# Kernel tuning notes

Hardware: AMD Instinct MI355X
Metric: run time of the kernel (lower is better)

The kernel has to match this reference:

```python
import jax, jax.numpy as jnp
import numpy as np

N = 50000   # nodes
E = 400000  # edges
H = 128     # num_hidden


def _glorot(key, shape):
    fan_in, fan_out = shape
    lim = float(np.sqrt(6.0 / (fan_in + fan_out)))
    return jax.random.uniform(key, shape, jnp.float32, -lim, lim)


def setup_inputs() -> dict:
    key = jax.random.key(0)
    ks = jax.random.split(key, 16)
    x = jax.random.normal(ks[0], (N, H), jnp.float32)
    pos = jax.random.normal(ks[1], (N, 3), jnp.float32)
    pe = jax.random.normal(ks[2], (N, H), jnp.float32)
    send = jax.random.randint(ks[3], (E,), 0, N)
    # avoid self-loops so dist > 0 (torch.norm grad at 0 is NaN; same hazard in jax)
    off = jax.random.randint(ks[4], (E,), 1, N)
    rec = (send + off) % N
    edge_index = jnp.stack([send, rec]).astype(jnp.int64)
    # message_mlp: Linear(4H+1, H) -> SiLU -> Linear(H, H) -> SiLU
    W1 = _glorot(ks[5], (4 * H + 1, H)); b1 = jnp.zeros((H,), jnp.float32)
    W2 = _glorot(ks[6], (H, H));          b2 = jnp.zeros((H,), jnp.float32)
    # message_mlp_pos: Linear(2H+1, H) -> Tanh -> Linear(H, H) -> Tanh
    Wp1 = _glorot(ks[7], (2 * H + 1, H)); bp1 = jnp.zeros((H,), jnp.float32)
    Wp2 = _glorot(ks[8], (H, H));          bp2 = jnp.zeros((H,), jnp.float32)
    return {"x": x, "pos": pos, "pe": pe, "edge_index": edge_index,
            "W1": W1, "b1": b1, "W2": W2, "b2": b2,
            "Wp1": Wp1, "bp1": bp1, "Wp2": Wp2, "bp2": bp2}


def reference(x, pos, pe, edge_index, W1, b1, W2, b2, Wp1, bp1, Wp2, bp2):
    send, rec = edge_index[0], edge_index[1]
    # gather node + pe features along edges
    dist = jnp.linalg.norm(pos[send] - pos[rec], axis=1, keepdims=True)  # [E,1]
    state = jnp.concatenate([x[send], pe[send], x[rec], pe[rec], dist], axis=1)  # [E,4H+1]
    state_pe = jnp.concatenate([pe[send], pe[rec], dist], axis=1)                 # [E,2H+1]
    # edge MLPs
    msg = jax.nn.silu(jax.nn.silu(state @ W1 + b1) @ W2 + b2)      # [E,H]
    msg_pe = jnp.tanh(jnp.tanh(state_pe @ Wp1 + bp1) @ Wp2 + bp2)  # [E,H]
    # scatter_add aggregate to receiving nodes
    aggr = jax.ops.segment_sum(msg, rec, num_segments=x.shape[0])
    aggr_pe = jax.ops.segment_sum(msg_pe, rec, num_segments=x.shape[0])
    # residual updates
    return x + aggr, pe + aggr_pe
```

## Files before the change

kernel.cpp:

```cpp
#include <hip/hip_runtime.h>
#include <stdint.h>

#define N_NODES 50000
#define NE      400000
#define HDIM    128
#define MPAD    50048
#define TE      128
#define NTILE   (NE / TE)
#define SCAN_BS 512
#define SCAN_NB 98

typedef __attribute__((ext_vector_type(8))) short bf16x8;
typedef __attribute__((ext_vector_type(4))) float f32x4;

__device__ __forceinline__ ushort f2b(float f) {
    uint32_t u = __float_as_uint(f);
    uint32_t r = (u + 0x7fffu + ((u >> 16) & 1u)) >> 16;
    return (ushort)r;
}
__device__ __forceinline__ float b2f(ushort s) {
    return __uint_as_float(((uint32_t)s) << 16);
}

__device__ __forceinline__ float silu_f(float x) {
    return x * __builtin_amdgcn_rcpf(1.f + __expf(-x));
}
__device__ __forceinline__ float tanh_f(float x) {
    return fmaf(-2.f, __builtin_amdgcn_rcpf(1.f + __expf(2.f * x)), 1.f);
}

__global__ void k_prep_nodes(const float4* __restrict__ x, const float4* __restrict__ pe,
                             ushort* __restrict__ Xc, float4* __restrict__ out) {
    int idx = blockIdx.x * 256 + threadIdx.x;
    int row = idx >> 6;
    int cq  = idx & 63;
    float4 v = make_float4(0.f, 0.f, 0.f, 0.f);
    if (row < N_NODES) {
        if (cq < 32) { v = x[row * 32 + cq];          out[row * 32 + cq] = v; }
        else         { v = pe[row * 32 + (cq - 32)];  out[N_NODES * 32 + row * 32 + (cq - 32)] = v; }
    }
    ushort r[4] = { f2b(v.x), f2b(v.y), f2b(v.z), f2b(v.w) };
    *(uint2*)(Xc + (size_t)row * 256 + cq * 4) = *(const uint2*)r;
}

__global__ void k_prep_w(const float* __restrict__ W1, const float* __restrict__ Wp1,
                         const float* __restrict__ W2, const float* __restrict__ Wp2,
                         ushort* __restrict__ WcT, ushort* __restrict__ W2t,
                         ushort* __restrict__ Wp2t, float* __restrict__ w1d,
                         float* __restrict__ wp1d) {
    int b = blockIdx.x, t = threadIdx.x;
    if (b < 512) {
        int n = b, k = t;
        float v;
        if (n < 128)       v = W1[k * HDIM + n];
        else if (n < 256)  v = W1[(256 + k) * HDIM + (n - 128)];
        else if (n < 384)  v = (k < 128) ? 0.f : Wp1[(k - 128) * HDIM + (n - 256)];
        else               v = (k < 128) ? 0.f : Wp1[k * HDIM + (n - 384)];
        WcT[n * 256 + k] = f2b(v);
    } else if (b < 640) {
        if (t < 128) { int n = b - 512; W2t[n * HDIM + t] = f2b(W2[t * HDIM + n]); }
    } else if (b < 768) {
        if (t < 128) { int n = b - 640; Wp2t[n * HDIM + t] = f2b(Wp2[t * HDIM + n]); }
    } else {
        if (t < 128) w1d[t] = W1[512 * HDIM + t];
        else if (t < 256) wp1d[t - 128] = Wp1[256 * HDIM + (t - 128)];
    }
}

__global__ void k_hist(const int* __restrict__ eidx, int* __restrict__ cnt) {
    int e = blockIdx.x * 256 + threadIdx.x;
    if (e < NE) atomicAdd(&cnt[eidx[NE + e]], 1);
}

__global__ __launch_bounds__(SCAN_BS) void k_scan1(const int* __restrict__ cnt,
                                                   int* __restrict__ locs,
                                                   int* __restrict__ sums) {
    __shared__ int sh[SCAN_BS];
    int tid = threadIdx.x;
    int i = blockIdx.x * SCAN_BS + tid;
    int v = (i < N_NODES) ? cnt[i] : 0;
    sh[tid] = v;
    __syncthreads();
    for (int off = 1; off < SCAN_BS; off <<= 1) {
        int t = (tid >= off) ? sh[tid - off] : 0;
        __syncthreads();
        sh[tid] += t;
        __syncthreads();
    }
    locs[i] = sh[tid];
    if (tid == SCAN_BS - 1) sums[blockIdx.x] = sh[tid];
}

__global__ void k_scan2(int* __restrict__ sums) {
    __shared__ int sh[128];
    int tid = threadIdx.x;
    sh[tid] = (tid < SCAN_NB) ? sums[tid] : 0;
    __syncthreads();
    for (int off = 1; off < 128; off <<= 1) {
        int t = (tid >= off) ? sh[tid - off] : 0;
        __syncthreads();
        sh[tid] += t;
        __syncthreads();
    }
    if (tid < SCAN_NB) sums[tid] = sh[tid];
}

__global__ __launch_bounds__(SCAN_BS) void k_scan3(const int* __restrict__ cnt,
                                                   const int* __restrict__ locs,
                                                   const int* __restrict__ sums,
                                                   int* __restrict__ start,
                                                   int* __restrict__ cursor) {
    int tid = threadIdx.x, b = blockIdx.x;
    int i = b * SCAN_BS + tid;
    if (i > N_NODES) return;
    int base = b ? sums[b - 1] : 0;
    int v = (i < N_NODES) ? cnt[i] : 0;
    int ex = base + locs[i] - v;
    start[i] = ex;
    if (i < N_NODES) cursor[i] = ex;
}

__global__ void k_place(const int* __restrict__ eidx, const float* __restrict__ pos,
                        int* __restrict__ cursor, int* __restrict__ sendS,
                        int* __restrict__ recS, float* __restrict__ distS) {
    int e = blockIdx.x * 256 + threadIdx.x;
    if (e >= NE) return;
    int s = eidx[e], r = eidx[NE + e];
    int p = atomicAdd(&cursor[r], 1);
    sendS[p] = s; recS[p] = r;
    float dx = pos[s * 3 + 0] - pos[r * 3 + 0];
    float dy = pos[s * 3 + 1] - pos[r * 3 + 1];
    float dz = pos[s * 3 + 2] - pos[r * 3 + 2];
    distS[p] = sqrtf(dx * dx + dy * dy + dz * dz);
}

__global__ __launch_bounds__(128) void k_segmeta(const int* __restrict__ recS,
                                                 const int* __restrict__ startA,
                                                 const int* __restrict__ cntA,
                                                 uint32_t* __restrict__ tileSegs,
                                                 int* __restrict__ segCnt) {
    __shared__ int sR[128];
    __shared__ int sFlag[128];
    __shared__ int sStart[129];
    int tid = threadIdx.x;
    int t0 = blockIdx.x * 128;
    sR[tid] = recS[t0 + tid];
    __syncthreads();
    int f = (tid == 0) || (sR[tid] != sR[tid - 1]);
    sFlag[tid] = f;
    __syncthreads();
    for (int off = 1; off < 128; off <<= 1) {
        int v = (tid >= off) ? sFlag[tid - off] : 0;
        __syncthreads();
        sFlag[tid] += v;
        __syncthreads();
    }
    int nSeg = sFlag[127];
    if (f) sStart[sFlag[tid] - 1] = tid;
    if (tid == 0) { sStart[nSeg] = 128; segCnt[blockIdx.x] = nSeg; }
    __syncthreads();
    if (f) {
        int seg = sFlag[tid] - 1;
        int r0 = tid;
        int len = sStart[seg + 1] - r0;
        int n = sR[r0];
        int g0 = t0 + r0;
        int st = startA[n];
        uint32_t interior = (g0 == st) && (g0 + len == st + cntA[n]);
        tileSegs[(size_t)blockIdx.x * 128 + seg] =
            (uint32_t)r0 | ((uint32_t)(len - 1) << 7) | (interior << 14) | ((uint32_t)n << 16);
    }
}

__global__ __launch_bounds__(256) void k_node_gemm(const ushort* __restrict__ Xc,
                                                   const ushort* __restrict__ WcT,
                                                   ushort* __restrict__ Pn) {
    const int m0 = blockIdx.y * 128;
    const int n0 = blockIdx.x * 128;
    const int wave = threadIdx.x >> 6;
    const int lane = threadIdx.x & 63;
    const int l15 = lane & 15, quad = lane >> 4;
    const int qr = (wave >> 1) * 64, qc = (wave & 1) * 64;

    f32x4 acc[4][4];
#pragma unroll
    for (int i = 0; i < 4; i++)
#pragma unroll
        for (int j = 0; j < 4; j++) acc[i][j] = (f32x4){0.f, 0.f, 0.f, 0.f};

#pragma unroll
    for (int s = 0; s < 8; s++) {
        const int k0 = s * 32 + quad * 8;
        bf16x8 a[4], b[4];
#pragma unroll
        for (int rg = 0; rg < 4; rg++) {
            int row = m0 + qr + rg * 16 + l15;
            a[rg] = *(const bf16x8*)(Xc + row * 256 + k0);
        }
#pragma unroll
        for (int cg = 0; cg < 4; cg++) {
            int nn = n0 + qc + cg * 16 + l15;
            b[cg] = *(const bf16x8*)(WcT + nn * 256 + k0);
        }
#pragma unroll
        for (int rg = 0; rg < 4; rg++)
#pragma unroll
            for (int cg = 0; cg < 4; cg++)
                acc[rg][cg] = __builtin_amdgcn_mfma_f32_16x16x32_bf16(a[rg], b[cg], acc[rg][cg], 0, 0, 0);
    }

#pragma unroll
    for (int rg = 0; rg < 4; rg++)
#pragma unroll
        for (int cg = 0; cg < 4; cg++) {
            int col = n0 + qc + cg * 16 + l15;
            int rowb = m0 + qr + rg * 16 + quad * 4;
#pragma unroll
            for (int r = 0; r < 4; r++)
                Pn[(size_t)(rowb + r) * 512 + col] = f2b(acc[rg][cg][r]);
        }
}

__global__ __launch_bounds__(256, 4) void k_fused(
    const ushort* __restrict__ Pn,
    const int* __restrict__ sendS, const int* __restrict__ recS,
    const float* __restrict__ distS,
    const uint32_t* __restrict__ tileSegs, const int* __restrict__ segCntA,
    const float* __restrict__ w1d, const float* __restrict__ wp1d,
    const float* __restrict__ b1, const float* __restrict__ bp1,
    const ushort* __restrict__ W2t, const ushort* __restrict__ Wp2t,
    const float* __restrict__ b2, const float* __restrict__ bp2,
    const float* __restrict__ x, const float* __restrict__ pe,
    float* __restrict__ out)
{
    __shared__ __align__(16) ushort sA[TE * 128];
    __shared__ int sS[TE];
    __shared__ int sR[TE];
    __shared__ float sD[TE];
    __shared__ uint32_t sSeg[TE];

    const int tid = threadIdx.x;
    const int tile = blockIdx.x;
    const int p = blockIdx.y;
    const int t0 = tile * TE;

    if (tid < TE) {
        sS[tid] = sendS[t0 + tid];
        sR[tid] = recS[t0 + tid];
        sD[tid] = distS[t0 + tid];
    } else {
        sSeg[tid - TE] = tileSegs[(size_t)tile * TE + (tid - TE)];
    }
    const int nSeg = segCntA[tile];

    const int g = tid >> 4, c = tid & 15;
    const float* wd = p ? wp1d : w1d;
    const float* bb = p ? bp1 : b1;
    float4 wv0 = *(const float4*)(wd + c * 8);
    float4 wv1 = *(const float4*)(wd + c * 8 + 4);
    float4 bv0 = *(const float4*)(bb + c * 8);
    float4 bv1 = *(const float4*)(bb + c * 8 + 4);
    float wva[8] = { wv0.x, wv0.y, wv0.z, wv0.w, wv1.x, wv1.y, wv1.z, wv1.w };
    float bva[8] = { bv0.x, bv0.y, bv0.z, bv0.w, bv1.x, bv1.y, bv1.z, bv1.w };
    __syncthreads();

    {
        const ushort* PnS = Pn + p * 256 + c * 8;
        const ushort* PnR = Pn + p * 256 + 128 + c * 8;
        uint4 us[8], ur[8];
#pragma unroll
        for (int e = 0; e < 8; e++) {
            int el = g * 8 + e;
            us[e] = *(const uint4*)(PnS + (size_t)sS[el] * 512);
            ur[e] = *(const uint4*)(PnR + (size_t)sR[el] * 512);
        }
#define L1_BODY(ACT)                                                        \
        for (int e = 0; e < 8; e++) {                                       \
            int el = g * 8 + e;                                             \
            float d = sD[el];                                               \
            const ushort* pus = (const ushort*)&us[e];                      \
            const ushort* pur = (const ushort*)&ur[e];                      \
            ushort res[8];                                                  \
            _Pragma("unroll")                                               \
            for (int j = 0; j < 8; j++) {                                   \
                float v = b2f(pus[j]) + b2f(pur[j]) + d * wva[j] + bva[j];  \
                res[j] = f2b(ACT(v));                                       \
            }                                                               \
            *(uint4*)(sA + el * 128 + ((c ^ (el & 15)) * 8)) = *(const uint4*)res; \
        }
        if (p) {
#pragma unroll
            L1_BODY(tanh_f)
        } else {
#pragma unroll
            L1_BODY(silu_f)
        }
#undef L1_BODY
    }
    __syncthreads();

    const int wave = tid >> 6, lane = tid & 63;
    const int l15 = lane & 15, quad = lane >> 4;
    const ushort* Wt = p ? Wp2t : W2t;

    f32x4 acc[2][8];
#pragma unroll
    for (int rg = 0; rg < 2; rg++)
#pragma unroll
        for (int cg = 0; cg < 8; cg++) acc[rg][cg] = (f32x4){0.f, 0.f, 0.f, 0.f};

#pragma unroll
    for (int s4 = 0; s4 < 4; s4++) {
        int cidx = s4 * 4 + quad;
        int row0 = wave * 32 + l15;
        bf16x8 a0 = *(const bf16x8*)(sA + row0 * 128 + ((cidx ^ l15) * 8));
        bf16x8 a1 = *(const bf16x8*)(sA + (row0 + 16) * 128 + ((cidx ^ l15) * 8));
        int k0 = cidx * 8;
#pragma unroll
        for (int cg = 0; cg < 8; cg++) {
            bf16x8 b = *(const bf16x8*)(Wt + (cg * 16 + l15) * HDIM + k0);
            acc[0][cg] = __builtin_amdgcn_mfma_f32_16x16x32_bf16(a0, b, acc[0][cg], 0, 0, 0);
            acc[1][cg] = __builtin_amdgcn_mfma_f32_16x16x32_bf16(a1, b, acc[1][cg], 0, 0, 0);
        }
    }
    __syncthreads();

    const float* bb2 = p ? bp2 : b2;
#define EPI_BODY(ACT)                                                       \
    for (int rg = 0; rg < 2; rg++) {                                        \
        int rowb = wave * 32 + rg * 16 + quad * 4;                          \
        _Pragma("unroll")                                                   \
        for (int cg = 0; cg < 8; cg++) {                                    \
            int col = cg * 16 + l15;                                        \
            float bias = bb2[col];                                          \
            _Pragma("unroll")                                               \
            for (int r = 0; r < 4; r++) {                                   \
                float v = acc[rg][cg][r] + bias;                            \
                sA[(rowb + r) * 128 + col] = f2b(ACT(v));                   \
            }                                                               \
        }                                                                   \
    }
    if (p) {
#pragma unroll
        EPI_BODY(tanh_f)
    } else {
#pragma unroll
        EPI_BODY(silu_f)
    }
#undef EPI_BODY
    __syncthreads();

    const float* basep = p ? pe : x;
    float* outb = out + (size_t)p * N_NODES * HDIM;
    for (int task = tid; task < nSeg * 64; task += 256) {
        int seg = task >> 6, cp = task & 63;
        uint32_t wseg = sSeg[seg];
        int r0  = wseg & 127;
        int len = ((wseg >> 7) & 127) + 1;
        int n   = wseg >> 16;
        float a0 = 0.f, a1 = 0.f;
        for (int rr = r0; rr < r0 + len; rr++) {
            unsigned int u = *(const unsigned int*)&sA[rr * 128 + cp * 2];
            a0 += b2f((ushort)(u & 0xffffu));
            a1 += b2f((ushort)(u >> 16));
        }
        float* op = outb + (size_t)n * HDIM + cp * 2;
        if ((wseg >> 14) & 1) {
            float2 bv = *(const float2*)(basep + (size_t)n * HDIM + cp * 2);
            *(float2*)op = make_float2(bv.x + a0, bv.y + a1);
        } else {
            atomicAdd(op, a0);
            atomicAdd(op + 1, a1);
        }
    }
}

extern "C" void kernel_launch(void* const* d_in, const int* in_sizes, int n_in,
                              void* d_out, int out_size, void* d_ws, size_t ws_size,
                              hipStream_t stream) {
    const float* x   = (const float*)d_in[0];
    const float* pos = (const float*)d_in[1];
    const float* pe  = (const float*)d_in[2];
    const int* eidx  = (const int*)d_in[3];
    const float* W1  = (const float*)d_in[4];
    const float* b1  = (const float*)d_in[5];
    const float* W2  = (const float*)d_in[6];
    const float* b2  = (const float*)d_in[7];
    const float* Wp1 = (const float*)d_in[8];
    const float* bp1 = (const float*)d_in[9];
    const float* Wp2 = (const float*)d_in[10];
    const float* bp2 = (const float*)d_in[11];
    float* out = (float*)d_out;

    char* w = (char*)d_ws;
    size_t off = 0;
    ushort* Xc   = (ushort*)(w + off); off += (size_t)MPAD * 256 * 2;
    ushort* Pn   = (ushort*)(w + off); off += (size_t)MPAD * 512 * 2;
    ushort* WcT  = (ushort*)(w + off); off += 512 * 256 * 2;
    ushort* W2t  = (ushort*)(w + off); off += 32768;
    ushort* Wp2t = (ushort*)(w + off); off += 32768;
    float*  w1d  = (float*)(w + off);  off += 2048;
    float*  wp1d = (float*)(w + off);  off += 2048;
    int* cnt     = (int*)(w + off);    off += 200704;
    int* startA  = (int*)(w + off);    off += 200704;
    int* cursor  = (int*)(w + off);    off += 200704;
    int* locs    = (int*)(w + off);    off += 200704;
    int* sums    = (int*)(w + off);    off += 512;
    int* sendS   = (int*)(w + off);    off += (size_t)NE * 4;
    int* recS    = (int*)(w + off);    off += (size_t)NE * 4;
    float* distS = (float*)(w + off);  off += (size_t)NE * 4;
    uint32_t* tileSegs = (uint32_t*)(w + off); off += (size_t)NTILE * 128 * 4;
    int* segCntA = (int*)(w + off);    off += (size_t)NTILE * 4;

    hipMemsetAsync(cnt, 0, (N_NODES + 1) * sizeof(int), stream);
    k_hist<<<(NE + 255) / 256, 256, 0, stream>>>(eidx, cnt);
    k_scan1<<<SCAN_NB, SCAN_BS, 0, stream>>>(cnt, locs, sums);
    k_scan2<<<1, 128, 0, stream>>>(sums);
    k_scan3<<<SCAN_NB, SCAN_BS, 0, stream>>>(cnt, locs, sums, startA, cursor);
    k_place<<<(NE + 255) / 256, 256, 0, stream>>>(eidx, pos, cursor, sendS, recS, distS);
    k_segmeta<<<NTILE, 128, 0, stream>>>(recS, startA, cnt, tileSegs, segCntA);

    k_prep_w<<<769, 256, 0, stream>>>(W1, Wp1, W2, Wp2, WcT, W2t, Wp2t, w1d, wp1d);
    k_prep_nodes<<<MPAD / 4, 256, 0, stream>>>((const float4*)x, (const float4*)pe,
                                               Xc, (float4*)out);

    dim3 ggrid(4, MPAD / 128);
    k_node_gemm<<<ggrid, 256, 0, stream>>>(Xc, WcT, Pn);

    dim3 fgrid(NTILE, 2);
    k_fused<<<fgrid, 256, 0, stream>>>(Pn, sendS, recS, distS, tileSegs, segCntA,
                                       w1d, wp1d, b1, bp1, W2t, Wp2t, b2, bp2,
                                       x, pe, out);
}
```

Baseline: 387.1 us.

## Skip redundant output init for fully covered nodes and drop fused-kernel LDS staging

Adds a per-node coverage flag computed in the scan pass, so prep_nodes only writes the residual base into out for nodes whose edges are not fully contained in one tile. Fully covered nodes get their output written directly with base+sum by the fused kernel. The fused kernel also stops staging send/rec/dist/segment metadata in shared memory and drops the initial barrier, loading indices straight into registers and reading segment words from global. Occupancy hint raised from 4 to 5 blocks per CU. This trades shared-memory traffic and a sync for more register pressure and repeated global reads of segment words.

```diff
diff --git a/kernel.cpp b/kernel.cpp
--- a/kernel.cpp
+++ b/kernel.cpp
@@ -30,14 +30,16 @@
 }
 
 __global__ void k_prep_nodes(const float4* __restrict__ x, const float4* __restrict__ pe,
+                             const int* __restrict__ cov,
                              ushort* __restrict__ Xc, float4* __restrict__ out) {
     int idx = blockIdx.x * 256 + threadIdx.x;
     int row = idx >> 6;
     int cq  = idx & 63;
     float4 v = make_float4(0.f, 0.f, 0.f, 0.f);
     if (row < N_NODES) {
-        if (cq < 32) { v = x[row * 32 + cq];          out[row * 32 + cq] = v; }
-        else         { v = pe[row * 32 + (cq - 32)];  out[N_NODES * 32 + row * 32 + (cq - 32)] = v; }
+        bool wr = (cov[row] == 0);
+        if (cq < 32) { v = x[row * 32 + cq];          if (wr) out[row * 32 + cq] = v; }
+        else         { v = pe[row * 32 + (cq - 32)];  if (wr) out[N_NODES * 32 + row * 32 + (cq - 32)] = v; }
     }
     ushort r[4] = { f2b(v.x), f2b(v.y), f2b(v.z), f2b(v.w) };
     *(uint2*)(Xc + (size_t)row * 256 + cq * 4) = *(const uint2*)r;
@@ -109,7 +111,8 @@
                                                    const int* __restrict__ locs,
                                                    const int* __restrict__ sums,
                                                    int* __restrict__ start,
-                                                   int* __restrict__ cursor) {
+                                                   int* __restrict__ cursor,
+                                                   int* __restrict__ nodeCov) {
     int tid = threadIdx.x, b = blockIdx.x;
     int i = b * SCAN_BS + tid;
     if (i > N_NODES) return;
@@ -117,7 +120,11 @@
     int v = (i < N_NODES) ? cnt[i] : 0;
     int ex = base + locs[i] - v;
     start[i] = ex;
-    if (i < N_NODES) cursor[i] = ex;
+    if (i < N_NODES) {
+        cursor[i] = ex;
+        int covered = (v > 0) && ((ex >> 7) == ((ex + v - 1) >> 7));
+        nodeCov[i] = covered;
+    }
 }
 
 __global__ void k_place(const int* __restrict__ eidx, const float* __restrict__ pos,
@@ -221,7 +228,7 @@
         }
 }
 
-__global__ __launch_bounds__(256, 4) void k_fused(
+__global__ __launch_bounds__(256, 5) void k_fused(
     const ushort* __restrict__ Pn,
     const int* __restrict__ sendS, const int* __restrict__ recS,
     const float* __restrict__ distS,
@@ -234,26 +241,26 @@
     float* __restrict__ out)
 {
     __shared__ __align__(16) ushort sA[TE * 128];
-    __shared__ int sS[TE];
-    __shared__ int sR[TE];
-    __shared__ float sD[TE];
-    __shared__ uint32_t sSeg[TE];
 
     const int tid = threadIdx.x;
     const int tile = blockIdx.x;
     const int p = blockIdx.y;
     const int t0 = tile * TE;
-
-    if (tid < TE) {
-        sS[tid] = sendS[t0 + tid];
-        sR[tid] = recS[t0 + tid];
-        sD[tid] = distS[t0 + tid];
-    } else {
-        sSeg[tid - TE] = tileSegs[(size_t)tile * TE + (tid - TE)];
-    }
     const int nSeg = segCntA[tile];
 
     const int g = tid >> 4, c = tid & 15;
+
+    const int e0 = t0 + g * 8;
+    int4 sv0 = *(const int4*)(sendS + e0);
+    int4 sv1 = *(const int4*)(sendS + e0 + 4);
+    int4 rv0 = *(const int4*)(recS + e0);
+    int4 rv1 = *(const int4*)(recS + e0 + 4);
+    float4 dv0 = *(const float4*)(distS + e0);
+    float4 dv1 = *(const float4*)(distS + e0 + 4);
+    int se[8] = { sv0.x, sv0.y, sv0.z, sv0.w, sv1.x, sv1.y, sv1.z, sv1.w };
+    int re[8] = { rv0.x, rv0.y, rv0.z, rv0.w, rv1.x, rv1.y, rv1.z, rv1.w };
+    float de[8] = { dv0.x, dv0.y, dv0.z, dv0.w, dv1.x, dv1.y, dv1.z, dv1.w };
+
     const float* wd = p ? wp1d : w1d;
     const float* bb = p ? bp1 : b1;
     float4 wv0 = *(const float4*)(wd + c * 8);
@@ -262,7 +269,6 @@
     float4 bv1 = *(const float4*)(bb + c * 8 + 4);
     float wva[8] = { wv0.x, wv0.y, wv0.z, wv0.w, wv1.x, wv1.y, wv1.z, wv1.w };
     float bva[8] = { bv0.x, bv0.y, bv0.z, bv0.w, bv1.x, bv1.y, bv1.z, bv1.w };
-    __syncthreads();
 
     {
         const ushort* PnS = Pn + p * 256 + c * 8;
@@ -270,14 +276,13 @@
         uint4 us[8], ur[8];
 #pragma unroll
         for (int e = 0; e < 8; e++) {
-            int el = g * 8 + e;
-            us[e] = *(const uint4*)(PnS + (size_t)sS[el] * 512);
-            ur[e] = *(const uint4*)(PnR + (size_t)sR[el] * 512);
+            us[e] = *(const uint4*)(PnS + (size_t)se[e] * 512);
+            ur[e] = *(const uint4*)(PnR + (size_t)re[e] * 512);
         }
 #define L1_BODY(ACT)                                                        \
         for (int e = 0; e < 8; e++) {                                       \
             int el = g * 8 + e;                                             \
-            float d = sD[el];                                               \
+            float d = de[e];                                                \
             const ushort* pus = (const ushort*)&us[e];                      \
             const ushort* pur = (const ushort*)&ur[e];                      \
             ushort res[8];                                                  \
@@ -352,9 +357,10 @@
 
     const float* basep = p ? pe : x;
     float* outb = out + (size_t)p * N_NODES * HDIM;
+    const uint32_t* segp = tileSegs + (size_t)tile * TE;
     for (int task = tid; task < nSeg * 64; task += 256) {
         int seg = task >> 6, cp = task & 63;
-        uint32_t wseg = sSeg[seg];
+        uint32_t wseg = segp[seg];
         int r0  = wseg & 127;
         int len = ((wseg >> 7) & 127) + 1;
         int n   = wseg >> 16;
@@ -411,18 +417,19 @@
     float* distS = (float*)(w + off);  off += (size_t)NE * 4;
     uint32_t* tileSegs = (uint32_t*)(w + off); off += (size_t)NTILE * 128 * 4;
     int* segCntA = (int*)(w + off);    off += (size_t)NTILE * 4;
+    int* nodeCov = (int*)(w + off);    off += 200704;
 
     hipMemsetAsync(cnt, 0, (N_NODES + 1) * sizeof(int), stream);
     k_hist<<<(NE + 255) / 256, 256, 0, stream>>>(eidx, cnt);
     k_scan1<<<SCAN_NB, SCAN_BS, 0, stream>>>(cnt, locs, sums);
     k_scan2<<<1, 128, 0, stream>>>(sums);
-    k_scan3<<<SCAN_NB, SCAN_BS, 0, stream>>>(cnt, locs, sums, startA, cursor);
+    k_scan3<<<SCAN_NB, SCAN_BS, 0, stream>>>(cnt, locs, sums, startA, cursor, nodeCov);
     k_place<<<(NE + 255) / 256, 256, 0, stream>>>(eidx, pos, cursor, sendS, recS, distS);
     k_segmeta<<<NTILE, 128, 0, stream>>>(recS, startA, cnt, tileSegs, segCntA);
 
     k_prep_w<<<769, 256, 0, stream>>>(W1, Wp1, W2, Wp2, WcT, W2t, Wp2t, w1d, wp1d);
     k_prep_nodes<<<MPAD / 4, 256, 0, stream>>>((const float4*)x, (const float4*)pe,
-                                               Xc, (float4*)out);
+                                               nodeCov, Xc, (float4*)out);
 
     dim3 ggrid(4, MPAD / 128);
     k_node_gemm<<<ggrid, 256, 0, stream>>>(Xc, WcT, Pn);
```

New measurement: 476.0 us. 23.0% more time.
